# Kernel optimization log

Hardware: AMD Instinct MI355X
Metric: run time of the kernel (lower is better)

## Reference

```python
import jax, jax.numpy as jnp
import numpy as np

H_LAT = 64   # latent height (original_shape H)
W_LAT = 64   # latent width  (original_shape W)
COND_LEN = 77  # text tokens per regional condition


def _resize_nearest_exact(m, H, W):
    # matches torch F.interpolate(mode='nearest-exact') for a 2D mask
    h0, w0 = m.shape
    ih = jnp.floor((jnp.arange(H) + 0.5) * (h0 / H)).astype(jnp.int32)
    iw = jnp.floor((jnp.arange(W) + 0.5) * (w0 / W)).astype(jnp.int32)
    return m[ih][:, iw]


def setup_inputs() -> dict:
    key = jax.random.key(0)
    kq, kk, kv, km = jax.random.split(key, 4)
    b, qlen, inner = 2, H_LAT * W_LAT, 512
    klen = 4 * COND_LEN  # 4 regions x 77 tokens
    q = jax.random.normal(kq, (b, qlen, inner), dtype=jnp.float32)
    k = jax.random.normal(kk, (b, klen, inner), dtype=jnp.float32)
    v = jax.random.normal(kv, (b, klen, inner), dtype=jnp.float32)
    dd_masks = jax.random.uniform(km, (4, 32, 32), dtype=jnp.float32)
    # ensure full spatial coverage (region 0 = global) so no softmax row is all-masked
    dd_masks = dd_masks.at[0].set(1.0)
    return {"q": q, "k": k, "v": v, "dd_masks": dd_masks, "heads": 8}


def reference(q, k, v, dd_masks, heads):
    b, qlen, inner = q.shape
    dh = inner // heads
    # [b, heads, seq, dh]
    qh = q.reshape(b, qlen, heads, dh).transpose(0, 2, 1, 3)
    kh = k.reshape(b, -1, heads, dh).transpose(0, 2, 1, 3)
    vh = v.reshape(b, -1, heads, dh).transpose(0, 2, 1, 3)

    # build DenseDiffusion mask: each region mask resized to HxW, flattened,
    # and repeated over that region's COND_LEN key columns
    R = dd_masks.shape[0]
    resized = jax.vmap(lambda m: _resize_nearest_exact(m, H_LAT, W_LAT))(dd_masks)  # [R,H,W]
    flat = resized.reshape(R, H_LAT * W_LAT).T            # [HW, R]
    masks = jnp.repeat(flat, COND_LEN, axis=1)            # [HW, R*COND_LEN]
    mask_bool = masks > 0.5                               # [HW, klen]
    mask_scale = (H_LAT * W_LAT) / jnp.sum(masks, axis=0, keepdims=True)  # [1, klen]

    scale = 1.0 / np.sqrt(dh).astype(np.float32)
    attn = jnp.einsum('bhqd,bhkd->bhqk', qh, kh) * scale  # [b,h,HW,klen]
    attn = attn * mask_scale                              # broadcast over b,h,q
    attn = jnp.where(mask_bool, attn, -jnp.inf)
    w = jax.nn.softmax(attn, axis=-1)
    out = jnp.einsum('bhqk,bhkd->bhqd', w, vh)
    return out.transpose(0, 2, 1, 3).reshape(b, qlen, heads * dh)
```

## Files before the change

### kernel.cpp

```cpp
#include <hip/hip_runtime.h>
#include <hip/hip_bf16.h>

typedef __attribute__((ext_vector_type(8))) short short8;
typedef __attribute__((ext_vector_type(4))) float floatx4;

#define HW_TOK 4096
#define KLEN 308
#define KPAD 320
#define DH 64
#define INNER 512
#define KSTR 72
#define VSTR 328
#define PSTR 72
#define NWAVE 8

__device__ __forceinline__ unsigned short f2bf(float f) {
    union { float f; unsigned u; } x; x.f = f;
    unsigned u = x.u;
    return (unsigned short)((u + 0x7FFFu + ((u >> 16) & 1u)) >> 16);
}

__global__ __launch_bounds__(512, 2)
void dd_attn_kernel(const float* __restrict__ q,
                    const float* __restrict__ k,
                    const float* __restrict__ v,
                    const float* __restrict__ dd,
                    float* __restrict__ out) {
    __shared__ unsigned short Klds[KPAD][KSTR];
    __shared__ unsigned short Vt[DH][VSTR];
    __shared__ unsigned short Pw[NWAVE][2][16][PSTR];
    __shared__ float rscale_s[4];

    const int tid  = threadIdx.x;
    const int lane = tid & 63;
    const int wave = tid >> 6;
    const int quad = lane >> 4;
    const int l15  = lane & 15;

    const int bid = blockIdx.x;
    const int bh  = bid >> 4;
    const int grp = bid & 15;
    const int b = bh >> 3;
    const int h = bh & 7;

    const float* qp = q + (size_t)b * HW_TOK * INNER + h * DH;
    const float* kp = k + (size_t)b * KLEN * INNER + h * DH;
    const float* vp = v + (size_t)b * KLEN * INNER + h * DH;
    float* op = out + (size_t)b * HW_TOK * INNER + h * DH;

    for (int e = tid; e < KPAD * 32; e += 512) {
        int row = e >> 5, d2 = e & 31;
        float2 f = make_float2(0.f, 0.f);
        if (row < KLEN) f = *(const float2*)(kp + (size_t)row * INNER + 2 * d2);
        *(unsigned*)&Klds[row][2 * d2] = ((unsigned)f2bf(f.y) << 16) | f2bf(f.x);
    }
    for (int e = tid; e < KLEN * 32; e += 512) {
        int col = e >> 5, d2 = e & 31;
        float2 f = *(const float2*)(vp + (size_t)col * INNER + 2 * d2);
        Vt[2 * d2][col]     = f2bf(f.x);
        Vt[2 * d2 + 1][col] = f2bf(f.y);
    }
    for (int e = tid; e < DH * 12; e += 512) {
        int d = e / 12, c = e % 12;
        Vt[d][KLEN + c] = 0;
    }
    if (wave < 4) {
        float p = 0.f;
        #pragma unroll
        for (int i = 0; i < 16; ++i) p += dd[wave * 1024 + lane + 64 * i];
        #pragma unroll
        for (int off = 32; off >= 1; off >>= 1) p += __shfl_xor(p, off);
        if (lane == 0) rscale_s[wave] = 4096.0f / (4.0f * p);
    }
    __syncthreads();

    const float rsv[4] = {rscale_s[0], rscale_s[1], rscale_s[2], rscale_s[3]};

    for (int it = 0; it < 2; ++it) {
        const int q0 = (grp * 16 + wave * 2 + it) * 16;

        const float* qr = qp + (size_t)(q0 + l15) * INNER + quad * 8;
        float4 f0 = *(const float4*)(qr);
        float4 f1 = *(const float4*)(qr + 4);
        float4 f2 = *(const float4*)(qr + 32);
        float4 f3 = *(const float4*)(qr + 36);
        short8 a0, a1;
        a0[0]=(short)f2bf(f0.x); a0[1]=(short)f2bf(f0.y); a0[2]=(short)f2bf(f0.z); a0[3]=(short)f2bf(f0.w);
        a0[4]=(short)f2bf(f1.x); a0[5]=(short)f2bf(f1.y); a0[6]=(short)f2bf(f1.z); a0[7]=(short)f2bf(f1.w);
        a1[0]=(short)f2bf(f2.x); a1[1]=(short)f2bf(f2.y); a1[2]=(short)f2bf(f2.z); a1[3]=(short)f2bf(f2.w);
        a1[4]=(short)f2bf(f3.x); a1[5]=(short)f2bf(f3.y); a1[6]=(short)f2bf(f3.z); a1[7]=(short)f2bf(f3.w);

        floatx4 acc[20];
        #pragma unroll
        for (int nt = 0; nt < 20; ++nt) {
            int col = nt * 16 + l15;
            short8 b0 = *(const short8*)&Klds[col][quad * 8];
            short8 b1 = *(const short8*)&Klds[col][32 + quad * 8];
            floatx4 c = {0.f, 0.f, 0.f, 0.f};
            c = __builtin_amdgcn_mfma_f32_16x16x32_bf16(a0, b0, c, 0, 0, 0);
            c = __builtin_amdgcn_mfma_f32_16x16x32_bf16(a1, b1, c, 0, 0, 0);
            acc[nt] = c;
        }

        float coef[4][4];
        #pragma unroll
        for (int r = 0; r < 4; ++r) {
            int qrow = q0 + quad * 4 + r;
            int mi = (qrow >> 7) * 32 + ((qrow & 63) >> 1);
            #pragma unroll
            for (int rg = 0; rg < 4; ++rg) {
                float mv = dd[rg * 1024 + mi];
                coef[r][rg] = (mv > 0.5f) ? 0.125f * rsv[rg] : -1.0f;
            }
        }

        float mx[4] = {-INFINITY, -INFINITY, -INFINITY, -INFINITY};
        #pragma unroll
        for (int nt = 0; nt < 20; ++nt) {
            #pragma unroll
            for (int r = 0; r < 4; ++r) {
                float c;
                if      (nt <  4) c = coef[r][0];
                else if (nt == 4) c = (l15 < 13) ? coef[r][0] : coef[r][1];
                else if (nt <  9) c = coef[r][1];
                else if (nt == 9) c = (l15 < 10) ? coef[r][1] : coef[r][2];
                else if (nt < 14) c = coef[r][2];
                else if (nt ==14) c = (l15 <  7) ? coef[r][2] : coef[r][3];
                else if (nt < 19) c = coef[r][3];
                else              c = (l15 <  4) ? coef[r][3] : -1.0f;
                float sv = (c > 0.f) ? acc[nt][r] * c : -INFINITY;
                acc[nt][r] = sv;
                mx[r] = fmaxf(mx[r], sv);
            }
        }
        #pragma unroll
        for (int off = 1; off < 16; off <<= 1) {
            #pragma unroll
            for (int r = 0; r < 4; ++r) mx[r] = fmaxf(mx[r], __shfl_xor(mx[r], off));
        }

        float sm[4] = {0.f, 0.f, 0.f, 0.f};
        #pragma unroll
        for (int nt = 0; nt < 20; ++nt) {
            #pragma unroll
            for (int r = 0; r < 4; ++r) {
                float p = __expf(acc[nt][r] - mx[r]);
                acc[nt][r] = p;
                sm[r] += p;
            }
        }
        #pragma unroll
        for (int off = 1; off < 16; off <<= 1) {
            #pragma unroll
            for (int r = 0; r < 4; ++r) sm[r] += __shfl_xor(sm[r], off);
        }
        float inv[4];
        #pragma unroll
        for (int r = 0; r < 4; ++r) inv[r] = 1.0f / sm[r];

        floatx4 oacc[4] = {{0.f,0.f,0.f,0.f},{0.f,0.f,0.f,0.f},{0.f,0.f,0.f,0.f},{0.f,0.f,0.f,0.f}};
        #pragma unroll
        for (int c5 = 0; c5 < 5; ++c5) {
            const int buf = c5 & 1;
            #pragma unroll
            for (int nt2 = 0; nt2 < 4; ++nt2) {
                int nt = c5 * 4 + nt2;
                #pragma unroll
                for (int r = 0; r < 4; ++r)
                    Pw[wave][buf][quad * 4 + r][nt2 * 16 + l15] = f2bf(acc[nt][r]);
            }
            #pragma unroll
            for (int ks = 0; ks < 2; ++ks) {
                short8 pa = *(const short8*)&Pw[wave][buf][l15][ks * 32 + quad * 8];
                #pragma unroll
                for (int n = 0; n < 4; ++n) {
                    short8 bv = *(const short8*)&Vt[n * 16 + l15][c5 * 64 + ks * 32 + quad * 8];
                    oacc[n] = __builtin_amdgcn_mfma_f32_16x16x32_bf16(pa, bv, oacc[n], 0, 0, 0);
                }
            }
        }

        #pragma unroll
        for (int n = 0; n < 4; ++n) {
            #pragma unroll
            for (int r = 0; r < 4; ++r) {
                op[(size_t)(q0 + quad * 4 + r) * INNER + n * 16 + l15] = oacc[n][r] * inv[r];
            }
        }
    }
}

extern "C" void kernel_launch(void* const* d_in, const int* in_sizes, int n_in,
                              void* d_out, int out_size, void* d_ws, size_t ws_size,
                              hipStream_t stream) {
    const float* q  = (const float*)d_in[0];
    const float* k  = (const float*)d_in[1];
    const float* v  = (const float*)d_in[2];
    const float* dd = (const float*)d_in[3];
    float* out = (float*)d_out;
    dd_attn_kernel<<<dim3(256), dim3(512), 0, stream>>>(q, k, v, dd, out);
}
```

Before: 108.8 us.

## Transpose attention MFMAs, swizzle LDS, use online softmax and double grid size

Computes S^T = K·Q^T and O^T = V^T·P^T so each lane owns one query row. Softmax reductions become two cross-quad shuffles, and P is handed to the PV MFMA through register shuffles instead of an LDS round trip. K and V are stored in XOR-swizzled, unpadded LDS to avoid bank conflicts. Softmax now runs online over two key chunks, and each block handles 128 queries instead of 256, so the grid doubles to 512 blocks. Outputs are written as float4. The trade-off is that K/V staging is repeated across twice as many blocks, and the extra per-chunk rescaling adds work.

```diff
diff --git a/kernel.cpp b/kernel.cpp
--- a/kernel.cpp
+++ b/kernel.cpp
@@ -6,18 +6,19 @@
 
 #define HW_TOK 4096
 #define KLEN 308
-#define KPAD 320
 #define DH 64
 #define INNER 512
-#define KSTR 72
-#define VSTR 328
-#define PSTR 72
-#define NWAVE 8
+
+#define VBASE (KLEN * 64)
+#define LDS_TOTAL (VBASE + DH * 320)
 
 __device__ __forceinline__ unsigned short f2bf(float f) {
     union { float f; unsigned u; } x; x.f = f;
     unsigned u = x.u;
     return (unsigned short)((u + 0x7FFFu + ((u >> 16) & 1u)) >> 16);
+}
+__device__ __forceinline__ unsigned pk2bf(float a, float b) {
+    return ((unsigned)f2bf(b) << 16) | (unsigned)f2bf(a);
 }
 
 __global__ __launch_bounds__(512, 2)
@@ -26,167 +27,176 @@
                     const float* __restrict__ v,
                     const float* __restrict__ dd,
                     float* __restrict__ out) {
-    __shared__ unsigned short Klds[KPAD][KSTR];
-    __shared__ unsigned short Vt[DH][VSTR];
-    __shared__ unsigned short Pw[NWAVE][2][16][PSTR];
-    __shared__ float rscale_s[4];
+    __shared__ unsigned short KV[LDS_TOTAL];
 
     const int tid  = threadIdx.x;
     const int lane = tid & 63;
     const int wave = tid >> 6;
     const int quad = lane >> 4;
     const int l15  = lane & 15;
+    const int kxor = l15 & 7;
 
     const int bid = blockIdx.x;
-    const int bh  = bid >> 4;
-    const int grp = bid & 15;
-    const int b = bh >> 3;
-    const int h = bh & 7;
+    const int bh  = bid >> 5;
+    const int grp = bid & 31;
+    const int b = bh >> 3, h = bh & 7;
 
     const float* qp = q + (size_t)b * HW_TOK * INNER + h * DH;
     const float* kp = k + (size_t)b * KLEN * INNER + h * DH;
     const float* vp = v + (size_t)b * KLEN * INNER + h * DH;
     float* op = out + (size_t)b * HW_TOK * INNER + h * DH;
 
-    for (int e = tid; e < KPAD * 32; e += 512) {
+    for (int e = tid; e < KLEN * 32; e += 512) {
         int row = e >> 5, d2 = e & 31;
-        float2 f = make_float2(0.f, 0.f);
-        if (row < KLEN) f = *(const float2*)(kp + (size_t)row * INNER + 2 * d2);
-        *(unsigned*)&Klds[row][2 * d2] = ((unsigned)f2bf(f.y) << 16) | f2bf(f.x);
+        float2 f = *(const float2*)(kp + (size_t)row * INNER + 2 * d2);
+        int c = d2 >> 2;
+        int off = row * 64 + (((c ^ (row & 7)) << 3) | ((d2 & 3) << 1));
+        *(unsigned*)&KV[off] = pk2bf(f.x, f.y);
     }
     for (int e = tid; e < KLEN * 32; e += 512) {
         int col = e >> 5, d2 = e & 31;
         float2 f = *(const float2*)(vp + (size_t)col * INNER + 2 * d2);
-        Vt[2 * d2][col]     = f2bf(f.x);
-        Vt[2 * d2 + 1][col] = f2bf(f.y);
+        int c = col >> 3, c7 = col & 7;
+        int r0 = 2 * d2, r1 = r0 + 1;
+        KV[VBASE + r0 * 320 + (((c & ~7) | ((c ^ r0) & 7)) << 3) + c7] = f2bf(f.x);
+        KV[VBASE + r1 * 320 + (((c & ~7) | ((c ^ r1) & 7)) << 3) + c7] = f2bf(f.y);
     }
     for (int e = tid; e < DH * 12; e += 512) {
-        int d = e / 12, c = e % 12;
-        Vt[d][KLEN + c] = 0;
-    }
-    if (wave < 4) {
-        float p = 0.f;
-        #pragma unroll
-        for (int i = 0; i < 16; ++i) p += dd[wave * 1024 + lane + 64 * i];
-        #pragma unroll
-        for (int off = 32; off >= 1; off >>= 1) p += __shfl_xor(p, off);
-        if (lane == 0) rscale_s[wave] = 4096.0f / (4.0f * p);
-    }
+        int row = e / 12, col = 308 + e % 12;
+        int c = col >> 3, c7 = col & 7;
+        KV[VBASE + row * 320 + (((c & ~7) | ((c ^ row) & 7)) << 3) + c7] = 0;
+    }
+
+    float rsum = 0.f;
+    {
+        const float* dp = dd + quad * 1024 + l15 * 4;
+        #pragma unroll
+        for (int j = 0; j < 16; ++j) {
+            float4 f = *(const float4*)(dp + j * 64);
+            rsum += f.x + f.y + f.z + f.w;
+        }
+        #pragma unroll
+        for (int off = 1; off < 16; off <<= 1) rsum += __shfl_xor(rsum, off);
+    }
+    float rsc[4];
+    #pragma unroll
+    for (int r = 0; r < 4; ++r)
+        rsc[r] = 4096.0f / (4.0f * __shfl(rsum, r * 16 + l15));
+
     __syncthreads();
 
-    const float rsv[4] = {rscale_s[0], rscale_s[1], rscale_s[2], rscale_s[3]};
-
-    for (int it = 0; it < 2; ++it) {
-        const int q0 = (grp * 16 + wave * 2 + it) * 16;
-
-        const float* qr = qp + (size_t)(q0 + l15) * INNER + quad * 8;
-        float4 f0 = *(const float4*)(qr);
-        float4 f1 = *(const float4*)(qr + 4);
-        float4 f2 = *(const float4*)(qr + 32);
-        float4 f3 = *(const float4*)(qr + 36);
-        short8 a0, a1;
-        a0[0]=(short)f2bf(f0.x); a0[1]=(short)f2bf(f0.y); a0[2]=(short)f2bf(f0.z); a0[3]=(short)f2bf(f0.w);
-        a0[4]=(short)f2bf(f1.x); a0[5]=(short)f2bf(f1.y); a0[6]=(short)f2bf(f1.z); a0[7]=(short)f2bf(f1.w);
-        a1[0]=(short)f2bf(f2.x); a1[1]=(short)f2bf(f2.y); a1[2]=(short)f2bf(f2.z); a1[3]=(short)f2bf(f2.w);
-        a1[4]=(short)f2bf(f3.x); a1[5]=(short)f2bf(f3.y); a1[6]=(short)f2bf(f3.z); a1[7]=(short)f2bf(f3.w);
-
-        floatx4 acc[20];
-        #pragma unroll
-        for (int nt = 0; nt < 20; ++nt) {
-            int col = nt * 16 + l15;
-            short8 b0 = *(const short8*)&Klds[col][quad * 8];
-            short8 b1 = *(const short8*)&Klds[col][32 + quad * 8];
+    const int q0 = (grp * 8 + wave) * 16;
+    const int qrow = q0 + l15;
+
+    const float* qr = qp + (size_t)qrow * INNER + quad * 8;
+    float4 f0 = *(const float4*)(qr);
+    float4 f1 = *(const float4*)(qr + 4);
+    float4 f2 = *(const float4*)(qr + 32);
+    float4 f3 = *(const float4*)(qr + 36);
+    short8 qa0, qa1;
+    qa0[0]=(short)f2bf(f0.x); qa0[1]=(short)f2bf(f0.y); qa0[2]=(short)f2bf(f0.z); qa0[3]=(short)f2bf(f0.w);
+    qa0[4]=(short)f2bf(f1.x); qa0[5]=(short)f2bf(f1.y); qa0[6]=(short)f2bf(f1.z); qa0[7]=(short)f2bf(f1.w);
+    qa1[0]=(short)f2bf(f2.x); qa1[1]=(short)f2bf(f2.y); qa1[2]=(short)f2bf(f2.z); qa1[3]=(short)f2bf(f2.w);
+    qa1[4]=(short)f2bf(f3.x); qa1[5]=(short)f2bf(f3.y); qa1[6]=(short)f2bf(f3.z); qa1[7]=(short)f2bf(f3.w);
+
+    const int mi = (qrow >> 7) * 32 + ((qrow & 63) >> 1);
+    float coef[4];
+    #pragma unroll
+    for (int r = 0; r < 4; ++r)
+        coef[r] = (dd[r * 1024 + mi] > 0.5f) ? 0.125f * rsc[r] : -1.0f;
+
+    float m_run = -INFINITY, l_run = 0.f;
+    floatx4 oacc[4] = {{0,0,0,0},{0,0,0,0},{0,0,0,0},{0,0,0,0}};
+
+    #pragma unroll
+    for (int ch = 0; ch < 2; ++ch) {
+        floatx4 acc[10];
+        #pragma unroll
+        for (int t = 0; t < 10; ++t) {
+            int row = (ch * 10 + t) * 16 + l15;
+            short8 ka0 = *(const short8*)&KV[row * 64 + ((quad       ^ kxor) << 3)];
+            short8 ka1 = *(const short8*)&KV[row * 64 + (((4 + quad) ^ kxor) << 3)];
             floatx4 c = {0.f, 0.f, 0.f, 0.f};
-            c = __builtin_amdgcn_mfma_f32_16x16x32_bf16(a0, b0, c, 0, 0, 0);
-            c = __builtin_amdgcn_mfma_f32_16x16x32_bf16(a1, b1, c, 0, 0, 0);
-            acc[nt] = c;
-        }
-
-        float coef[4][4];
-        #pragma unroll
-        for (int r = 0; r < 4; ++r) {
-            int qrow = q0 + quad * 4 + r;
-            int mi = (qrow >> 7) * 32 + ((qrow & 63) >> 1);
-            #pragma unroll
-            for (int rg = 0; rg < 4; ++rg) {
-                float mv = dd[rg * 1024 + mi];
-                coef[r][rg] = (mv > 0.5f) ? 0.125f * rsv[rg] : -1.0f;
+            c = __builtin_amdgcn_mfma_f32_16x16x32_bf16(ka0, qa0, c, 0, 0, 0);
+            c = __builtin_amdgcn_mfma_f32_16x16x32_bf16(ka1, qa1, c, 0, 0, 0);
+            acc[t] = c;
+        }
+
+        float mloc = -INFINITY;
+        #pragma unroll
+        for (int t = 0; t < 10; ++t) {
+            #pragma unroll
+            for (int r = 0; r < 4; ++r) {
+                int kc = (ch * 10 + t) * 16 + quad * 4 + r;
+                float cf = (kc < 77) ? coef[0] : (kc < 154) ? coef[1]
+                         : (kc < 231) ? coef[2] : (kc < 308) ? coef[3] : -1.0f;
+                float sv = (cf > 0.f) ? acc[t][r] * cf : -INFINITY;
+                acc[t][r] = sv;
+                mloc = fmaxf(mloc, sv);
             }
         }
-
-        float mx[4] = {-INFINITY, -INFINITY, -INFINITY, -INFINITY};
-        #pragma unroll
-        for (int nt = 0; nt < 20; ++nt) {
+        mloc = fmaxf(mloc, __shfl_xor(mloc, 16));
+        mloc = fmaxf(mloc, __shfl_xor(mloc, 32));
+
+        float m_new = fmaxf(m_run, mloc);
+        float alpha = __expf(m_run - m_new);
+        float lloc = 0.f;
+        #pragma unroll
+        for (int t = 0; t < 10; ++t) {
             #pragma unroll
             for (int r = 0; r < 4; ++r) {
-                float c;
-                if      (nt <  4) c = coef[r][0];
-                else if (nt == 4) c = (l15 < 13) ? coef[r][0] : coef[r][1];
-                else if (nt <  9) c = coef[r][1];
-                else if (nt == 9) c = (l15 < 10) ? coef[r][1] : coef[r][2];
-                else if (nt < 14) c = coef[r][2];
-                else if (nt ==14) c = (l15 <  7) ? coef[r][2] : coef[r][3];
-                else if (nt < 19) c = coef[r][3];
-                else              c = (l15 <  4) ? coef[r][3] : -1.0f;
-                float sv = (c > 0.f) ? acc[nt][r] * c : -INFINITY;
-                acc[nt][r] = sv;
-                mx[r] = fmaxf(mx[r], sv);
+                float p = __expf(acc[t][r] - m_new);
+                acc[t][r] = p;
+                lloc += p;
             }
         }
-        #pragma unroll
-        for (int off = 1; off < 16; off <<= 1) {
-            #pragma unroll
-            for (int r = 0; r < 4; ++r) mx[r] = fmaxf(mx[r], __shfl_xor(mx[r], off));
-        }
-
-        float sm[4] = {0.f, 0.f, 0.f, 0.f};
-        #pragma unroll
-        for (int nt = 0; nt < 20; ++nt) {
-            #pragma unroll
-            for (int r = 0; r < 4; ++r) {
-                float p = __expf(acc[nt][r] - mx[r]);
-                acc[nt][r] = p;
-                sm[r] += p;
+        lloc += __shfl_xor(lloc, 16);
+        lloc += __shfl_xor(lloc, 32);
+        l_run = l_run * alpha + lloc;
+        m_run = m_new;
+        #pragma unroll
+        for (int n = 0; n < 4; ++n)
+            #pragma unroll
+            for (int r = 0; r < 4; ++r) oacc[n][r] *= alpha;
+
+        const int sl0 = ((quad & 1) << 5) + l15;
+        const int sl1 = sl0 + 16;
+        const bool hi = (quad >= 2);
+        #pragma unroll
+        for (int c32 = 0; c32 < 5; ++c32) {
+            floatx4 pA = acc[2 * c32];
+            floatx4 pB = acc[2 * c32 + 1];
+            unsigned uA0 = pk2bf(pA[0], pA[1]), uA1 = pk2bf(pA[2], pA[3]);
+            unsigned uB0 = pk2bf(pB[0], pB[1]), uB1 = pk2bf(pB[2], pB[3]);
+            unsigned xA0 = (unsigned)__shfl((int)uA0, sl0), xB0 = (unsigned)__shfl((int)uB0, sl0);
+            unsigned xA1 = (unsigned)__shfl((int)uA1, sl0), xB1 = (unsigned)__shfl((int)uB1, sl0);
+            unsigned yA0 = (unsigned)__shfl((int)uA0, sl1), yB0 = (unsigned)__shfl((int)uB0, sl1);
+            unsigned yA1 = (unsigned)__shfl((int)uA1, sl1), yB1 = (unsigned)__shfl((int)uB1, sl1);
+            union { short8 s; unsigned u[4]; } pu;
+            pu.u[0] = hi ? xB0 : xA0;
+            pu.u[1] = hi ? xB1 : xA1;
+            pu.u[2] = hi ? yB0 : yA0;
+            pu.u[3] = hi ? yB1 : yA1;
+            #pragma unroll
+            for (int n = 0; n < 4; ++n) {
+                int row = n * 16 + l15;
+                int c = ch * 20 + c32 * 4 + quad;
+                int cs = (c & ~7) | ((c ^ kxor) & 7);
+                short8 va = *(const short8*)&KV[VBASE + row * 320 + (cs << 3)];
+                oacc[n] = __builtin_amdgcn_mfma_f32_16x16x32_bf16(va, pu.s, oacc[n], 0, 0, 0);
             }
         }
-        #pragma unroll
-        for (int off = 1; off < 16; off <<= 1) {
-            #pragma unroll
-            for (int r = 0; r < 4; ++r) sm[r] += __shfl_xor(sm[r], off);
-        }
-        float inv[4];
-        #pragma unroll
-        for (int r = 0; r < 4; ++r) inv[r] = 1.0f / sm[r];
-
-        floatx4 oacc[4] = {{0.f,0.f,0.f,0.f},{0.f,0.f,0.f,0.f},{0.f,0.f,0.f,0.f},{0.f,0.f,0.f,0.f}};
-        #pragma unroll
-        for (int c5 = 0; c5 < 5; ++c5) {
-            const int buf = c5 & 1;
-            #pragma unroll
-            for (int nt2 = 0; nt2 < 4; ++nt2) {
-                int nt = c5 * 4 + nt2;
-                #pragma unroll
-                for (int r = 0; r < 4; ++r)
-                    Pw[wave][buf][quad * 4 + r][nt2 * 16 + l15] = f2bf(acc[nt][r]);
-            }
-            #pragma unroll
-            for (int ks = 0; ks < 2; ++ks) {
-                short8 pa = *(const short8*)&Pw[wave][buf][l15][ks * 32 + quad * 8];
-                #pragma unroll
-                for (int n = 0; n < 4; ++n) {
-                    short8 bv = *(const short8*)&Vt[n * 16 + l15][c5 * 64 + ks * 32 + quad * 8];
-                    oacc[n] = __builtin_amdgcn_mfma_f32_16x16x32_bf16(pa, bv, oacc[n], 0, 0, 0);
-                }
-            }
-        }
-
-        #pragma unroll
-        for (int n = 0; n < 4; ++n) {
-            #pragma unroll
-            for (int r = 0; r < 4; ++r) {
-                op[(size_t)(q0 + quad * 4 + r) * INNER + n * 16 + l15] = oacc[n][r] * inv[r];
-            }
-        }
+    }
+
+    const float inv = 1.0f / l_run;
+    #pragma unroll
+    for (int n = 0; n < 4; ++n) {
+        float4 o;
+        o.x = oacc[n][0] * inv;
+        o.y = oacc[n][1] * inv;
+        o.z = oacc[n][2] * inv;
+        o.w = oacc[n][3] * inv;
+        *(float4*)&op[(size_t)qrow * INNER + n * 16 + quad * 4] = o;
     }
 }
 
@@ -198,5 +208,5 @@
     const float* v  = (const float*)d_in[2];
     const float* dd = (const float*)d_in[3];
     float* out = (float*)d_out;
-    dd_attn_kernel<<<dim3(256), dim3(512), 0, stream>>>(q, k, v, dd, out);
-}
+    dd_attn_kernel<<<dim3(512), dim3(512), 0, stream>>>(q, k, v, dd, out);
+}
```

Result: faster. 105.1 us (-3.4%).
